# Kernel tuning notes

Measured on AMD Instinct MI355X. Metric: run time of the kernel, lower is better.

## Reference

```python
import jax, jax.numpy as jnp
import numpy as np

B, H, W, D, K = 16, 64, 64, 128, 4096


def setup_inputs() -> dict:
    key = jax.random.key(0)
    k1, k2 = jax.random.split(key)
    z = jax.random.normal(k1, (B, H, W, D), dtype=jnp.float32)
    emb = jax.random.normal(k2, (K, D), dtype=jnp.float32)
    return {"z": z, "emb": emb}


def reference(z, emb):
    # z: [B,H,W,D] pre-quantized features (channels-last, as in the torch code
    # after permute(0,2,3,1)); emb: [K,D] codebook.
    d = z.shape[-1]
    zf = z.reshape(-1, d)  # [N,D]
    # squared euclidean distances: ||z||^2 + ||e||^2 - 2 z.e
    dists = (jnp.sum(zf * zf, axis=1, keepdims=True)
             + jnp.sum(emb * emb, axis=1)
             - 2.0 * zf @ emb.T)  # [N,K]
    idx = jnp.argmin(dists, axis=1)  # [N]
    # one-hot @ emb in the original == direct gather (same math)
    z_q = jnp.take(emb, idx, axis=0).reshape(z.shape)  # [B,H,W,D]
    codebook_loss = jnp.mean((jax.lax.stop_gradient(z_q) - z) ** 2)
    commitment_loss = jnp.mean((z_q - jax.lax.stop_gradient(z)) ** 2)
    loss = codebook_loss + 0.25 * commitment_loss
    # straight-through estimator
    z_q_st = z + jax.lax.stop_gradient(z_q - z)
    z_q_out = jnp.transpose(z_q_st, (0, 3, 1, 2))  # [B,D,H,W]
    return z_q_out, loss
```

## Files before the change

### kernel.cpp

```cpp
#include <hip/hip_runtime.h>

#define NB 16
#define NH 64
#define NW 64
#define ND 128
#define NK 4096
#define NROWS (NB * NH * NW)
#define OUT_ELEMS (NB * ND * NH * NW)
#define MARGIN_F 0.10f

typedef _Float16 f16x8 __attribute__((ext_vector_type(8)));
typedef float f32x4 __attribute__((ext_vector_type(4)));

__device__ __forceinline__ unsigned short f2h(float x) {
    _Float16 h = (_Float16)x;
    return __builtin_bit_cast(unsigned short, h);
}
__device__ __forceinline__ unsigned long long pack_si(float s, int idx) {
    unsigned int u = __float_as_uint(s);
    unsigned int key = ((int)u < 0) ? ~u : (u | 0x80000000u);
    return ((unsigned long long)key << 32) | (unsigned int)idx;
}

__global__ void emb_prep_kernel(const float* __restrict__ emb,
                                float* __restrict__ enorm,
                                unsigned short* __restrict__ e_h) {
    int wave = (blockIdx.x * blockDim.x + threadIdx.x) >> 6;
    int lane = threadIdx.x & 63;
    if (wave >= NK) return;
    const float* e = emb + (size_t)wave * ND;
    float a = e[lane];
    float b = e[lane + 64];
    const int m = (wave & 7) << 3;
    e_h[(size_t)wave * ND + (lane ^ m)] = f2h(a);
    e_h[(size_t)wave * ND + ((lane + 64) ^ m)] = f2h(b);
    float s = a * a + b * b;
#pragma unroll
    for (int off = 32; off > 0; off >>= 1) s += __shfl_down(s, off, 64);
    if (lane == 0) enorm[wave] = s;
}

#define ZST 136

__global__ void
__attribute__((amdgpu_flat_work_group_size(256, 256)))
mfma_argmin_kernel(const float* __restrict__ z,
                   const unsigned short* __restrict__ e_h,
                   const float* __restrict__ enorm,
                   int* __restrict__ idx_out,
                   int* __restrict__ rcount,
                   int* __restrict__ rlist,
                   unsigned long long* __restrict__ rpart) {
    __shared__ alignas(16) unsigned short ubuf[2 * 64 * ND];
    __shared__ float redb1[2 * 64];
    __shared__ float redb2[2 * 64];
    __shared__ int   redi1[2 * 64];

    const int bid = blockIdx.x;
    const int rowbase = bid * 64;
    const int t = threadIdx.x;
    const int lane = t & 63;
    const int wid = __builtin_amdgcn_readfirstlane(t >> 6);

    const float4* zg = (const float4*)(z + (size_t)rowbase * ND);
#pragma unroll
    for (int q = 0; q < 8; q++) {
        int i = t + 256 * q;
        float4 v = zg[i];
        int r = i >> 5;
        int c4 = (i & 31) << 2;
        ushort4 hv = make_ushort4(f2h(v.x), f2h(v.y), f2h(v.z), f2h(v.w));
        *(ushort4*)&ubuf[r * ZST + c4] = hv;
    }
    __syncthreads();

    const int quad = lane >> 4;
    const int c = lane & 15;
    const int rh = wid >> 1;
    const int ch = wid & 1;

    f16x8 ar[2][4];
#pragma unroll
    for (int mi = 0; mi < 2; mi++)
#pragma unroll
        for (int kk = 0; kk < 4; kk++)
            ar[mi][kk] = *(const f16x8*)&ubuf[(rh * 32 + mi * 16 + c) * ZST + quad * 8 + kk * 32];
    __syncthreads();

#pragma unroll
    for (int j = 0; j < 4; j++) {
        int seg = (wid << 2) + j;
        __builtin_amdgcn_global_load_lds(
            (const unsigned int*)(e_h + seg * 512 + lane * 8),
            (unsigned int*)&ubuf[seg * 512], 16, 0, 0);
    }
    float en0 = enorm[ch * 32 + c];
    float en1 = enorm[ch * 32 + 16 + c];
    __syncthreads();

    const int bswz = (c & 7) << 3;
    const int bbase0 = (ch * 32 + c) * ND;

    float b1[2][4], b2[2][4];
    int i1[2][4];
#pragma unroll
    for (int mi = 0; mi < 2; mi++)
#pragma unroll
        for (int r = 0; r < 4; r++) { b1[mi][r] = -3.4e38f; b2[mi][r] = -3.4e38f; i1[mi][r] = 0; }

    for (int ts = 0; ts < NK / 64; ts++) {
        const int cur = ts & 1;
        const int curoff = cur << 13;

        float nen0 = 0.f, nen1 = 0.f;
        if (ts < NK / 64 - 1) {
            nen0 = enorm[(ts + 1) * 64 + ch * 32 + c];
            nen1 = enorm[(ts + 1) * 64 + ch * 32 + 16 + c];
            const unsigned short* gt = e_h + (size_t)(ts + 1) * (64 * ND);
#pragma unroll
            for (int j = 0; j < 4; j++) {
                int seg = (wid << 2) + j;
                __builtin_amdgcn_global_load_lds(
                    (const unsigned int*)(gt + seg * 512 + lane * 8),
                    (unsigned int*)&ubuf[(curoff ^ 8192) + seg * 512], 16, 0, 0);
            }
        }

        const float h0 = -0.5f * en0;
        const float h1 = -0.5f * en1;
        f32x4 acc[2][2];
#pragma unroll
        for (int mi = 0; mi < 2; mi++) {
            acc[mi][0] = (f32x4){h0, h0, h0, h0};
            acc[mi][1] = (f32x4){h1, h1, h1, h1};
        }

#pragma unroll
        for (int kk = 0; kk < 4; kk++) {
            const int doff = (quad * 8 + kk * 32) ^ bswz;
            f16x8 bv0 = *(const f16x8*)&ubuf[curoff + bbase0 + doff];
            f16x8 bv1 = *(const f16x8*)&ubuf[curoff + bbase0 + 16 * ND + doff];
            acc[0][0] = __builtin_amdgcn_mfma_f32_16x16x32_f16(ar[0][kk], bv0, acc[0][0], 0, 0, 0);
            acc[0][1] = __builtin_amdgcn_mfma_f32_16x16x32_f16(ar[0][kk], bv1, acc[0][1], 0, 0, 0);
            acc[1][0] = __builtin_amdgcn_mfma_f32_16x16x32_f16(ar[1][kk], bv0, acc[1][0], 0, 0, 0);
            acc[1][1] = __builtin_amdgcn_mfma_f32_16x16x32_f16(ar[1][kk], bv1, acc[1][1], 0, 0, 0);
        }

#pragma unroll
        for (int ni = 0; ni < 2; ni++) {
            const int n = ts * 64 + ch * 32 + ni * 16 + c;
#pragma unroll
            for (int mi = 0; mi < 2; mi++)
#pragma unroll
                for (int r = 0; r < 4; r++) {
                    float q = acc[mi][ni][r];
                    b2[mi][r] = fmaxf(b2[mi][r], fminf(b1[mi][r], q));
                    i1[mi][r] = (q > b1[mi][r]) ? n : i1[mi][r];
                    b1[mi][r] = fmaxf(b1[mi][r], q);
                }
        }

        __syncthreads();
        en0 = nen0;
        en1 = nen1;
    }

#pragma unroll
    for (int off = 1; off < 16; off <<= 1) {
#pragma unroll
        for (int mi = 0; mi < 2; mi++)
#pragma unroll
            for (int r = 0; r < 4; r++) {
                float ob1 = __shfl_xor(b1[mi][r], off, 64);
                float ob2 = __shfl_xor(b2[mi][r], off, 64);
                int oi1 = __shfl_xor(i1[mi][r], off, 64);
                float hi = fmaxf(b1[mi][r], ob1);
                float lo = fminf(b1[mi][r], ob1);
                b2[mi][r] = fmaxf(fmaxf(b2[mi][r], ob2), lo);
                i1[mi][r] = (ob1 > b1[mi][r]) ? oi1 : i1[mi][r];
                b1[mi][r] = hi;
            }
    }

    if (c == 0) {
#pragma unroll
        for (int mi = 0; mi < 2; mi++)
#pragma unroll
            for (int r = 0; r < 4; r++) {
                int rowl = rh * 32 + mi * 16 + quad * 4 + r;
                redb1[ch * 64 + rowl] = b1[mi][r];
                redb2[ch * 64 + rowl] = b2[mi][r];
                redi1[ch * 64 + rowl] = i1[mi][r];
            }
    }
    __syncthreads();

    if (t < 64) {
        float B1 = redb1[t], B2 = redb2[t];
        int I1 = redi1[t];
        float ob1 = redb1[64 + t];
        float ob2 = redb2[64 + t];
        int oi1 = redi1[64 + t];
        float hi = fmaxf(B1, ob1);
        float lo = fminf(B1, ob1);
        B2 = fmaxf(fmaxf(B2, ob2), lo);
        I1 = (ob1 > B1) ? oi1 : I1;
        B1 = hi;
        idx_out[rowbase + t] = I1;
        if (2.0f * (B1 - B2) < MARGIN_F) {
            rpart[rowbase + t] = ~0ull;
            int p = atomicAdd(rcount, 1);
            rlist[p] = rowbase + t;
        }
    }
}

#define RR 4
#define SC 512
#define CH 64

__global__ void __launch_bounds__(256, 2)
rescue_kernel(const float* __restrict__ z,
              const float* __restrict__ emb,
              const float* __restrict__ enorm,
              const int* __restrict__ rcount,
              const int* __restrict__ rlist,
              unsigned long long* __restrict__ rpart) {
    __shared__ float2 ze[64 * RR];
    __shared__ float2 es[64 * 65];
    __shared__ int ids[RR];

    const int t = threadIdx.x;
    const int cnt = *rcount;
    if (cnt == 0) return;
    const int ngrp = (cnt + RR - 1) / RR;
    const int nwork = ngrp * 8;

    const int r = t >> 6;
    const int cl = t & 63;

    for (int g = blockIdx.x; g < nwork; g += gridDim.x) {
        const int gi = g >> 3;
        const int slice = g & 7;

        if (t < RR) {
            int j = gi * RR + t;
            ids[t] = rlist[j < cnt ? j : cnt - 1];
        }
        __syncthreads();
        const int row = ids[r];
        ze[cl * RR + r] = ((const float2*)(z + (size_t)row * ND))[cl];

        unsigned long long bestp = ~0ull;
        const int kbase = slice * SC;

        for (int ch2 = 0; ch2 < SC / CH; ch2++) {
            __syncthreads();
#pragma unroll
            for (int q = 0; q < 16; q++) {
                int i = t + 256 * q;
                int code = i >> 6;
                int d2 = i & 63;
                float2 v = ((const float2*)(emb + (size_t)(kbase + ch2 * CH + code) * ND))[d2];
                es[d2 * 65 + code] = v;
            }
            __syncthreads();

            int k = kbase + ch2 * CH + cl;
            float a0 = 0.f, a1 = 0.f, a2 = 0.f, a3 = 0.f;
#pragma unroll
            for (int d2 = 0; d2 < 64; d2 += 2) {
                float2 zv0 = ze[d2 * RR + r];
                float2 ev0 = es[d2 * 65 + cl];
                float2 zv1 = ze[(d2 + 1) * RR + r];
                float2 ev1 = es[(d2 + 1) * 65 + cl];
                a0 = fmaf(zv0.x, ev0.x, a0);
                a1 = fmaf(zv0.y, ev0.y, a1);
                a2 = fmaf(zv1.x, ev1.x, a2);
                a3 = fmaf(zv1.y, ev1.y, a3);
            }
            float s = fmaf(-2.0f, (a0 + a1) + (a2 + a3), enorm[k]);
            unsigned long long p = pack_si(s, k);
            bestp = (p < bestp) ? p : bestp;
        }

#pragma unroll
        for (int off = 32; off > 0; off >>= 1) {
            unsigned long long o = __shfl_down(bestp, off, 64);
            bestp = (o < bestp) ? o : bestp;
        }
        if (cl == 0) atomicMin(&rpart[row], bestp);
        __syncthreads();
    }
}

__global__ void rescue_fin_kernel(const int* __restrict__ rcount,
                                  const int* __restrict__ rlist,
                                  const unsigned long long* __restrict__ rpart,
                                  int* __restrict__ idx_out) {
    const int cnt = *rcount;
    for (int i = blockIdx.x * blockDim.x + threadIdx.x; i < cnt;
         i += gridDim.x * blockDim.x) {
        int row = rlist[i];
        idx_out[row] = (int)(rpart[row] & 0xffffffffull);
    }
}

__global__ void out_kernel(const float* __restrict__ z,
                           const float* __restrict__ emb,
                           const int* __restrict__ idx,
                           float* __restrict__ out,
                           float* __restrict__ losspart) {
    __shared__ float zq[64 * 129];
    __shared__ int ids[64];
    __shared__ float redl[4];

    const int bid = blockIdx.x;
    const int b = bid >> 6;
    const int h = bid & 63;
    const int rowbase = bid * 64;
    const int t = threadIdx.x;

    if (t < 64) ids[t] = idx[rowbase + t];
    __syncthreads();

    const int d = t & 127;
    const int w0 = t >> 7;
    float lsum = 0.f;
#pragma unroll
    for (int wq = 0; wq < 32; wq++) {
        int w = w0 + 2 * wq;
        float e = emb[(size_t)ids[w] * ND + d];
        float zv = z[((size_t)(rowbase + w)) * ND + d];
        float df = e - zv;
        lsum = fmaf(df, df, lsum);
        zq[w * 129 + d] = e;
    }
#pragma unroll
    for (int off = 32; off > 0; off >>= 1) lsum += __shfl_down(lsum, off, 64);
    if ((t & 63) == 0) redl[t >> 6] = lsum;
    __syncthreads();
    if (t == 0) losspart[bid] = redl[0] + redl[1] + redl[2] + redl[3];

    const int w = t & 63;
    const int dq = t >> 6;
#pragma unroll
    for (int dd0 = 0; dd0 < 32; dd0++) {
        int dd = dq + 4 * dd0;
        out[(((size_t)b * ND + dd) * NH + h) * NW + w] = zq[w * 129 + dd];
    }
}

__global__ void loss_kernel(const float* __restrict__ losspart,
                            float* __restrict__ out) {
    __shared__ float redl[4];
    const int t = threadIdx.x;
    float s = 0.f;
#pragma unroll
    for (int i = 0; i < 4; i++) s += losspart[t + 256 * i];
#pragma unroll
    for (int off = 32; off > 0; off >>= 1) s += __shfl_down(s, off, 64);
    if ((t & 63) == 0) redl[t >> 6] = s;
    __syncthreads();
    if (t == 0) {
        float total = redl[0] + redl[1] + redl[2] + redl[3];
        out[OUT_ELEMS] = 1.25f * total / (float)OUT_ELEMS;
    }
}

extern "C" void kernel_launch(void* const* d_in, const int* in_sizes, int n_in,
                              void* d_out, int out_size, void* d_ws, size_t ws_size,
                              hipStream_t stream) {
    const float* z = (const float*)d_in[0];
    const float* emb = (const float*)d_in[1];
    float* out = (float*)d_out;

    char* ws = (char*)d_ws;
    int* ws_idx = (int*)ws;
    float* ws_enorm = (float*)(ws + (256 << 10));
    float* ws_losspart = (float*)(ws + (272 << 10));
    int* ws_rcount = (int*)(ws + (276 << 10));
    int* ws_rlist = (int*)(ws + (277 << 10));
    unsigned short* ws_eh = (unsigned short*)(ws + (533 << 10));
    unsigned long long* ws_rpart = (unsigned long long*)(ws + (1557 << 10));

    hipMemsetAsync(ws_rcount, 0, sizeof(int), stream);
    emb_prep_kernel<<<NK / 4, 256, 0, stream>>>(emb, ws_enorm, ws_eh);
    mfma_argmin_kernel<<<NROWS / 64, 256, 0, stream>>>(z, ws_eh, ws_enorm,
                                                       ws_idx, ws_rcount,
                                                       ws_rlist, ws_rpart);
    rescue_kernel<<<2048, 256, 0, stream>>>(z, emb, ws_enorm, ws_rcount,
                                            ws_rlist, ws_rpart);
    rescue_fin_kernel<<<64, 256, 0, stream>>>(ws_rcount, ws_rlist, ws_rpart,
                                              ws_idx);
    out_kernel<<<NB * NH, 256, 0, stream>>>(z, emb, ws_idx, out, ws_losspart);
    loss_kernel<<<1, 256, 0, stream>>>(ws_losspart, out);
}
```

Before: 307.9 us.

## Track top-3 candidates and resolve two-way ambiguities with a cheap pair kernel

```diff
diff --git a/kernel.cpp b/kernel.cpp
--- a/kernel.cpp
+++ b/kernel.cpp
@@ -50,11 +50,15 @@
                    int* __restrict__ idx_out,
                    int* __restrict__ rcount,
                    int* __restrict__ rlist,
-                   unsigned long long* __restrict__ rpart) {
+                   unsigned long long* __restrict__ rpart,
+                   int* __restrict__ pcount,
+                   int2* __restrict__ plist) {
     __shared__ alignas(16) unsigned short ubuf[2 * 64 * ND];
     __shared__ float redb1[2 * 64];
     __shared__ float redb2[2 * 64];
+    __shared__ float redb3[2 * 64];
     __shared__ int   redi1[2 * 64];
+    __shared__ int   redi2[2 * 64];
 
     const int bid = blockIdx.x;
     const int rowbase = bid * 64;
@@ -101,12 +105,15 @@
     const int bswz = (c & 7) << 3;
     const int bbase0 = (ch * 32 + c) * ND;
 
-    float b1[2][4], b2[2][4];
-    int i1[2][4];
+    float b1[2][4], b2[2][4], b3[2][4];
+    int i1[2][4], i2[2][4];
 #pragma unroll
     for (int mi = 0; mi < 2; mi++)
 #pragma unroll
-        for (int r = 0; r < 4; r++) { b1[mi][r] = -3.4e38f; b2[mi][r] = -3.4e38f; i1[mi][r] = 0; }
+        for (int r = 0; r < 4; r++) {
+            b1[mi][r] = -3.4e38f; b2[mi][r] = -3.4e38f; b3[mi][r] = -3.4e38f;
+            i1[mi][r] = 0; i2[mi][r] = 0;
+        }
 
     for (int ts = 0; ts < NK / 64; ts++) {
         const int cur = ts & 1;
@@ -154,6 +161,9 @@
 #pragma unroll
                 for (int r = 0; r < 4; r++) {
                     float q = acc[mi][ni][r];
+                    b3[mi][r] = fmaxf(b3[mi][r], fminf(b2[mi][r], q));
+                    i2[mi][r] = (q > b1[mi][r]) ? i1[mi][r]
+                              : ((q > b2[mi][r]) ? n : i2[mi][r]);
                     b2[mi][r] = fmaxf(b2[mi][r], fminf(b1[mi][r], q));
                     i1[mi][r] = (q > b1[mi][r]) ? n : i1[mi][r];
                     b1[mi][r] = fmaxf(b1[mi][r], q);
@@ -173,12 +183,22 @@
             for (int r = 0; r < 4; r++) {
                 float ob1 = __shfl_xor(b1[mi][r], off, 64);
                 float ob2 = __shfl_xor(b2[mi][r], off, 64);
+                float ob3 = __shfl_xor(b3[mi][r], off, 64);
                 int oi1 = __shfl_xor(i1[mi][r], off, 64);
-                float hi = fmaxf(b1[mi][r], ob1);
-                float lo = fminf(b1[mi][r], ob1);
-                b2[mi][r] = fmaxf(fmaxf(b2[mi][r], ob2), lo);
-                i1[mi][r] = (ob1 > b1[mi][r]) ? oi1 : i1[mi][r];
-                b1[mi][r] = hi;
+                int oi2 = __shfl_xor(i2[mi][r], off, 64);
+                bool f = ob1 > b1[mi][r];
+                float w2 = f ? ob2 : b2[mi][r];
+                float w3 = f ? ob3 : b3[mi][r];
+                float l1 = f ? b1[mi][r] : ob1;
+                float v2 = f ? b2[mi][r] : ob2;
+                int wi2 = f ? oi2 : i2[mi][r];
+                int li1 = f ? i1[mi][r] : oi1;
+                i1[mi][r] = f ? oi1 : i1[mi][r];
+                b1[mi][r] = fmaxf(b1[mi][r], ob1);
+                bool g = l1 > w2;
+                i2[mi][r] = g ? li1 : wi2;
+                b2[mi][r] = fmaxf(l1, w2);
+                b3[mi][r] = fmaxf(fmaxf(fminf(l1, w2), w3), v2);
             }
     }
 
@@ -190,27 +210,40 @@
                 int rowl = rh * 32 + mi * 16 + quad * 4 + r;
                 redb1[ch * 64 + rowl] = b1[mi][r];
                 redb2[ch * 64 + rowl] = b2[mi][r];
+                redb3[ch * 64 + rowl] = b3[mi][r];
                 redi1[ch * 64 + rowl] = i1[mi][r];
+                redi2[ch * 64 + rowl] = i2[mi][r];
             }
     }
     __syncthreads();
 
     if (t < 64) {
-        float B1 = redb1[t], B2 = redb2[t];
-        int I1 = redi1[t];
-        float ob1 = redb1[64 + t];
-        float ob2 = redb2[64 + t];
-        int oi1 = redi1[64 + t];
-        float hi = fmaxf(B1, ob1);
-        float lo = fminf(B1, ob1);
-        B2 = fmaxf(fmaxf(B2, ob2), lo);
-        I1 = (ob1 > B1) ? oi1 : I1;
-        B1 = hi;
+        float B1 = redb1[t], B2 = redb2[t], B3 = redb3[t];
+        int I1 = redi1[t], I2 = redi2[t];
+        float ob1 = redb1[64 + t], ob2 = redb2[64 + t], ob3 = redb3[64 + t];
+        int oi1 = redi1[64 + t], oi2 = redi2[64 + t];
+        bool f = ob1 > B1;
+        float w2 = f ? ob2 : B2;
+        float w3 = f ? ob3 : B3;
+        float l1 = f ? B1 : ob1;
+        float v2 = f ? B2 : ob2;
+        int wi2 = f ? oi2 : I2;
+        int li1 = f ? I1 : oi1;
+        I1 = f ? oi1 : I1;
+        B1 = fmaxf(B1, ob1);
+        bool g = l1 > w2;
+        I2 = g ? li1 : wi2;
+        B2 = fmaxf(l1, w2);
+        B3 = fmaxf(fmaxf(fminf(l1, w2), w3), v2);
+
         idx_out[rowbase + t] = I1;
-        if (2.0f * (B1 - B2) < MARGIN_F) {
+        if (2.0f * (B1 - B3) < MARGIN_F) {
             rpart[rowbase + t] = ~0ull;
             int p = atomicAdd(rcount, 1);
             rlist[p] = rowbase + t;
+        } else if (2.0f * (B1 - B2) < MARGIN_F) {
+            int p = atomicAdd(pcount, 1);
+            plist[p] = make_int2(rowbase + t, I2);
         }
     }
 }
@@ -306,6 +339,41 @@
     }
 }
 
+__global__ void pair_kernel(const float* __restrict__ z,
+                            const float* __restrict__ emb,
+                            const float* __restrict__ enorm,
+                            const int* __restrict__ pcount,
+                            const int2* __restrict__ plist,
+                            int* __restrict__ idx_out) {
+    const int cnt = *pcount;
+    const int lane = threadIdx.x & 63;
+    const int gw = (blockIdx.x * blockDim.x + threadIdx.x) >> 6;
+    const int nw = (gridDim.x * blockDim.x) >> 6;
+    for (int i = gw; i < cnt; i += nw) {
+        int2 p = plist[i];
+        const int row = p.x;
+        const int j2 = p.y;
+        const int j1 = idx_out[row];
+        float2 zv = ((const float2*)(z + (size_t)row * ND))[lane];
+        float2 e1 = ((const float2*)(emb + (size_t)j1 * ND))[lane];
+        float2 e2 = ((const float2*)(emb + (size_t)j2 * ND))[lane];
+        float d1 = zv.x * e1.x + zv.y * e1.y;
+        float d2 = zv.x * e2.x + zv.y * e2.y;
+#pragma unroll
+        for (int off = 32; off > 0; off >>= 1) {
+            d1 += __shfl_down(d1, off, 64);
+            d2 += __shfl_down(d2, off, 64);
+        }
+        if (lane == 0) {
+            float s1 = fmaf(-2.0f, d1, enorm[j1]);
+            float s2 = fmaf(-2.0f, d2, enorm[j2]);
+            unsigned long long p1 = pack_si(s1, j1);
+            unsigned long long p2 = pack_si(s2, j2);
+            idx_out[row] = (int)(((p2 < p1) ? p2 : p1) & 0xffffffffull);
+        }
+    }
+}
+
 __global__ void out_kernel(const float* __restrict__ z,
                            const float* __restrict__ emb,
                            const int* __restrict__ idx,
@@ -380,17 +448,22 @@
     float* ws_enorm = (float*)(ws + (256 << 10));
     float* ws_losspart = (float*)(ws + (272 << 10));
     int* ws_rcount = (int*)(ws + (276 << 10));
+    int* ws_pcount = ws_rcount + 1;
     int* ws_rlist = (int*)(ws + (277 << 10));
     unsigned short* ws_eh = (unsigned short*)(ws + (533 << 10));
     unsigned long long* ws_rpart = (unsigned long long*)(ws + (1557 << 10));
-
-    hipMemsetAsync(ws_rcount, 0, sizeof(int), stream);
+    int2* ws_plist = (int2*)(ws + (2069 << 10));
+
+    hipMemsetAsync(ws_rcount, 0, 2 * sizeof(int), stream);
     emb_prep_kernel<<<NK / 4, 256, 0, stream>>>(emb, ws_enorm, ws_eh);
     mfma_argmin_kernel<<<NROWS / 64, 256, 0, stream>>>(z, ws_eh, ws_enorm,
                                                        ws_idx, ws_rcount,
-                                                       ws_rlist, ws_rpart);
+                                                       ws_rlist, ws_rpart,
+                                                       ws_pcount, ws_plist);
     rescue_kernel<<<2048, 256, 0, stream>>>(z, emb, ws_enorm, ws_rcount,
                                             ws_rlist, ws_rpart);
+    pair_kernel<<<256, 256, 0, stream>>>(z, emb, ws_enorm, ws_pcount,
+                                         ws_plist, ws_idx);
     rescue_fin_kernel<<<64, 256, 0, stream>>>(ws_rcount, ws_rlist, ws_rpart,
                                               ws_idx);
     out_kernel<<<NB * NH, 256, 0, stream>>>(z, emb, ws_idx, out, ws_losspart);
```

Result: slower. 331.3 us (+7.6%).
